# Kernel optimization log

Hardware: AMD Instinct MI355X
Metric: run time of the kernel (lower is better)

Reference implementation:

```python
import jax, jax.numpy as jnp
import numpy as np

T = 2048      # sequence length (block_size)
C = 4096      # n_embd
H = 32        # n_head
KVH = 8       # n_kv_head
D = 128       # head_dim = n_embd // n_head
NEG_INF = -40000.0
ROPE_BASE = 10000.0


def setup_inputs() -> dict:
    key = jax.random.key(0)
    ks = jax.random.split(key, 5)
    x = jax.random.normal(ks[0], (T, C), jnp.float32)
    # nn.Linear weights stored as (in, out); y = x @ W. Small init for numerical sanity.
    Wq = jax.random.normal(ks[1], (C, H * D), jnp.float32) * 0.02
    Wk = jax.random.normal(ks[2], (C, KVH * D), jnp.float32) * 0.02
    Wv = jax.random.normal(ks[3], (C, KVH * D), jnp.float32) * 0.02
    Wo = jax.random.normal(ks[4], (C, C), jnp.float32) * 0.02
    # Standard LLaMA-style RoPE tables: (T, D)
    inv_freq = 1.0 / (ROPE_BASE ** (np.arange(0, D, 2, dtype=np.float32) / D))
    freqs = np.outer(np.arange(T, dtype=np.float32), inv_freq)  # (T, D/2)
    emb = np.concatenate([freqs, freqs], axis=-1)                # (T, D)
    cos = jnp.asarray(np.cos(emb), jnp.float32)
    sin = jnp.asarray(np.sin(emb), jnp.float32)
    # Additive causal mask (T, T): 0 on/below diagonal, neg_inf above.
    causal = np.tril(np.ones((T, T), dtype=bool))
    mask = jnp.where(jnp.asarray(causal), 0.0, NEG_INF).astype(jnp.float32)
    return {"x": x, "Wq": Wq, "Wk": Wk, "Wv": Wv, "Wo": Wo,
            "cos": cos, "sin": sin, "mask": mask}


def _rotate_half(u):
    u1, u2 = jnp.split(u, 2, axis=-1)
    return jnp.concatenate([-u2, u1], axis=-1)


def _apply_rope(u, cos, sin):
    # u: (heads, T, D); cos/sin: (T, D) broadcast over heads
    return u * cos + _rotate_half(u) * sin


def reference(x, Wq, Wk, Wv, Wo, cos, sin, mask):
    Tn = x.shape[0]
    q = (x @ Wq).reshape(Tn, H, D).transpose(1, 0, 2)      # (H, T, D)
    k = (x @ Wk).reshape(Tn, KVH, D).transpose(1, 0, 2)    # (KVH, T, D)
    v = (x @ Wv).reshape(Tn, KVH, D).transpose(1, 0, 2)    # (KVH, T, D)
    q = _apply_rope(q, cos, sin)
    k = _apply_rope(k, cos, sin)
    out_k, out_v = k, v
    # GQA expand: each kv head repeated contiguously H//KVH times
    rep = H // KVH
    ke = jnp.repeat(k, rep, axis=0)                         # (H, T, D)
    ve = jnp.repeat(v, rep, axis=0)                         # (H, T, D)
    # NOTE: no 1/sqrt(D) scaling in the original module
    att = jnp.einsum('htd,hsd->hts', q, ke) + mask          # (H, T, T)
    att = jax.nn.softmax(att, axis=-1)
    y = jnp.einsum('hts,hsd->htd', att, ve)                 # (H, T, D)
    y = y.transpose(1, 0, 2).reshape(Tn, C) @ Wo            # (T, C)
    return (y, out_k, out_v)
```

## Files before the change

### kernel.cpp

```cpp
#include <hip/hip_runtime.h>
#include <hip/hip_bf16.h>

#define T 2048
#define C 4096
#define H 32
#define KVH 8
#define D 128

typedef __bf16 bf16x8 __attribute__((ext_vector_type(8)));
typedef __bf16 bf16x4 __attribute__((ext_vector_type(4)));
typedef float floatx4 __attribute__((ext_vector_type(4)));

#define MFMA16 __builtin_amdgcn_mfma_f32_16x16x32_bf16

__device__ __forceinline__ void gemm_split_body(
    const float* __restrict__ A, const float* __restrict__ B,
    float* __restrict__ Cm, int N, int K, int row0, int col0) {
  __shared__ __bf16 Ah[128][40], Al[128][40], Bh[128][40], Bl[128][40];
  const int tid = threadIdx.x;
  const int lane = tid & 63;
  const int w = tid >> 6;
  const int n16 = lane & 15;
  const int quad = lane >> 4;
  const int wm = w >> 1, wn = w & 1;

  floatx4 acc[4][4];
#pragma unroll
  for (int mi = 0; mi < 4; ++mi)
#pragma unroll
    for (int ni = 0; ni < 4; ++ni) acc[mi][ni] = (floatx4){0.f, 0.f, 0.f, 0.f};

  const int ar = tid >> 3;
  const int ak = (tid & 7) * 4;
  const int bg = tid >> 7;
  const int bn = tid & 127;

  for (int k0 = 0; k0 < K; k0 += 32) {
#pragma unroll
    for (int p = 0; p < 4; ++p) {
      const int r = p * 32 + ar;
      const float4 av = *(const float4*)(A + (size_t)(row0 + r) * K + k0 + ak);
      bf16x4 h, l;
      h[0] = (__bf16)av.x; l[0] = (__bf16)(av.x - (float)h[0]);
      h[1] = (__bf16)av.y; l[1] = (__bf16)(av.y - (float)h[1]);
      h[2] = (__bf16)av.z; l[2] = (__bf16)(av.z - (float)h[2]);
      h[3] = (__bf16)av.w; l[3] = (__bf16)(av.w - (float)h[3]);
      *(bf16x4*)(&Ah[r][ak]) = h;
      *(bf16x4*)(&Al[r][ak]) = l;
    }
#pragma unroll
    for (int p = 0; p < 4; ++p) {
      const int kb = bg * 16 + p * 4;
      const float* bp = B + (size_t)(k0 + kb) * N + col0 + bn;
      const float f0 = bp[0];
      const float f1 = bp[(size_t)N];
      const float f2 = bp[(size_t)2 * N];
      const float f3 = bp[(size_t)3 * N];
      bf16x4 h, l;
      h[0] = (__bf16)f0; l[0] = (__bf16)(f0 - (float)h[0]);
      h[1] = (__bf16)f1; l[1] = (__bf16)(f1 - (float)h[1]);
      h[2] = (__bf16)f2; l[2] = (__bf16)(f2 - (float)h[2]);
      h[3] = (__bf16)f3; l[3] = (__bf16)(f3 - (float)h[3]);
      *(bf16x4*)(&Bh[bn][kb]) = h;
      *(bf16x4*)(&Bl[bn][kb]) = l;
    }
    __syncthreads();
    bf16x8 a_h[4], a_l[4], b_h[4], b_l[4];
#pragma unroll
    for (int mi = 0; mi < 4; ++mi) {
      a_h[mi] = *(const bf16x8*)(&Ah[wm * 64 + mi * 16 + n16][quad * 8]);
      a_l[mi] = *(const bf16x8*)(&Al[wm * 64 + mi * 16 + n16][quad * 8]);
    }
#pragma unroll
    for (int ni = 0; ni < 4; ++ni) {
      b_h[ni] = *(const bf16x8*)(&Bh[wn * 64 + ni * 16 + n16][quad * 8]);
      b_l[ni] = *(const bf16x8*)(&Bl[wn * 64 + ni * 16 + n16][quad * 8]);
    }
#pragma unroll
    for (int mi = 0; mi < 4; ++mi)
#pragma unroll
      for (int ni = 0; ni < 4; ++ni) {
        acc[mi][ni] = MFMA16(a_h[mi], b_h[ni], acc[mi][ni], 0, 0, 0);
        acc[mi][ni] = MFMA16(a_l[mi], b_h[ni], acc[mi][ni], 0, 0, 0);
        acc[mi][ni] = MFMA16(a_h[mi], b_l[ni], acc[mi][ni], 0, 0, 0);
      }
    __syncthreads();
  }
#pragma unroll
  for (int mi = 0; mi < 4; ++mi)
#pragma unroll
    for (int i = 0; i < 4; ++i) {
      const int r = row0 + wm * 64 + mi * 16 + quad * 4 + i;
      float* cp = Cm + (size_t)r * N + col0 + wn * 64 + n16;
#pragma unroll
      for (int ni = 0; ni < 4; ++ni) cp[ni * 16] = acc[mi][ni][i];
    }
}

__global__ __launch_bounds__(256) void gemm_split(
    const float* __restrict__ A, const float* __restrict__ B,
    float* __restrict__ Cm, int N, int K) {
  gemm_split_body(A, B, Cm, N, K, blockIdx.y * 128, blockIdx.x * 128);
}

__global__ __launch_bounds__(256) void gemm_kv(
    const float* __restrict__ A, const float* __restrict__ Bk,
    const float* __restrict__ Bv, float* __restrict__ Ck,
    float* __restrict__ Cv, int K) {
  const int bx = blockIdx.x;
  const float* Bp = (bx < 8) ? Bk : Bv;
  float* Cp = (bx < 8) ? Ck : Cv;
  gemm_split_body(A, Bp, Cp, KVH * D, K, blockIdx.y * 128, (bx & 7) * 128);
}

__global__ __launch_bounds__(256) void rope_kernel(
    float* __restrict__ q, float* __restrict__ k,
    const float* __restrict__ cosb,
    const float* __restrict__ sinb) {
  int idx = blockIdx.x * 256 + threadIdx.x;
  int total = T * (H + KVH) * (D / 2);
  if (idx >= total) return;
  int d = idx % (D / 2);
  int rest = idx / (D / 2);
  int head = rest % (H + KVH);
  int t = rest / (H + KVH);
  float cv = cosb[(size_t)t * D + d];
  float sv = sinb[(size_t)t * D + d];
  float* base;
  if (head < H) base = q + (size_t)t * (H * D) + head * D;
  else          base = k + (size_t)t * (KVH * D) + (head - H) * D;
  float u1 = base[d];
  float u2 = base[d + D / 2];
  base[d]         = u1 * cv - u2 * sv;
  base[d + D / 2] = u2 * cv + u1 * sv;
}

__global__ __launch_bounds__(256) void convert_k(
    const float* __restrict__ k_ws, float* __restrict__ out_k,
    __bf16* __restrict__ khi, __bf16* __restrict__ klo) {
  int idx = blockIdx.x * 256 + threadIdx.x;
  if (idx >= KVH * T * D) return;
  int d = idx & (D - 1);
  int t = (idx >> 7) & (T - 1);
  int kvh = idx >> 18;
  float f = k_ws[(size_t)t * (KVH * D) + kvh * D + d];
  out_k[idx] = f;
  __bf16 hi = (__bf16)f;
  khi[idx] = hi;
  klo[idx] = (__bf16)(f - (float)hi);
}

__global__ __launch_bounds__(256) void convert_v(
    const float* __restrict__ v_ws, float* __restrict__ out_v,
    __bf16* __restrict__ vt) {
  __shared__ __bf16 tile[64][65];
  const int t0 = blockIdx.x * 64;
  const int d0 = blockIdx.y * 64;
  const int kvh = blockIdx.z;
#pragma unroll
  for (int p = 0; p < 16; ++p) {
    int i = p * 256 + threadIdx.x;
    int r = i >> 6;
    int c = i & 63;
    float f = v_ws[(size_t)(t0 + r) * (KVH * D) + kvh * D + d0 + c];
    out_v[((size_t)kvh * T + t0 + r) * D + d0 + c] = f;
    tile[r][c] = (__bf16)f;
  }
  __syncthreads();
#pragma unroll
  for (int p = 0; p < 16; ++p) {
    int i = p * 256 + threadIdx.x;
    int dd = i >> 6;
    int tt = i & 63;
    vt[((size_t)kvh * D + d0 + dd) * T + t0 + tt] = tile[tt][dd];
  }
}

struct StageRegs { bf16x8 k0, k1, l0, l1, v0, v1; };

__device__ __forceinline__ void stage_load(
    StageRegs& s, const __bf16* __restrict__ Kh, const __bf16* __restrict__ Kl,
    const __bf16* __restrict__ Vt, int j0, int tid) {
  const int kr = tid >> 4, kj = (tid & 15) * 8;
  s.k0 = *(const bf16x8*)(Kh + (size_t)(j0 + kr) * D + kj);
  s.k1 = *(const bf16x8*)(Kh + (size_t)(j0 + kr + 16) * D + kj);
  s.l0 = *(const bf16x8*)(Kl + (size_t)(j0 + kr) * D + kj);
  s.l1 = *(const bf16x8*)(Kl + (size_t)(j0 + kr + 16) * D + kj);
  const int vd = tid >> 2, vj = (tid & 3) * 8;
  s.v0 = *(const bf16x8*)(Vt + (size_t)vd * T + j0 + vj);
  s.v1 = *(const bf16x8*)(Vt + (size_t)(vd + 64) * T + j0 + vj);
}

__device__ __forceinline__ void stage_write(
    const StageRegs& s, __bf16* __restrict__ KhL, __bf16* __restrict__ KlL,
    __bf16* __restrict__ VL, int tid) {
  const int kr = tid >> 4, kj = (tid & 15) * 8;
  *(bf16x8*)(KhL + kr * 136 + kj) = s.k0;
  *(bf16x8*)(KhL + (kr + 16) * 136 + kj) = s.k1;
  *(bf16x8*)(KlL + kr * 136 + kj) = s.l0;
  *(bf16x8*)(KlL + (kr + 16) * 136 + kj) = s.l1;
  const int vd = tid >> 2, vj = (tid & 3) * 8;
  *(bf16x8*)(VL + vd * 40 + vj) = s.v0;
  *(bf16x8*)(VL + (vd + 64) * 40 + vj) = s.v1;
}

__device__ __forceinline__ void softmax_pv(
    floatx4 s0, floatx4 s1,
    const __bf16* __restrict__ VT, __bf16* __restrict__ Pw,
    floatx4* __restrict__ O, float* __restrict__ m_i, float* __restrict__ l_i,
    int j0, int r_base, int n16, int quad) {
  if (j0 + 31 > r_base) {
#pragma unroll
    for (int i = 0; i < 4; ++i) {
      int r = r_base + quad * 4 + i;
      if (j0 + n16 > r) s0[i] = -INFINITY;
      if (j0 + 16 + n16 > r) s1[i] = -INFINITY;
    }
  }
  float p0[4], p1[4];
#pragma unroll
  for (int i = 0; i < 4; ++i) {
    float mt = fmaxf(s0[i], s1[i]);
    mt = fmaxf(mt, __shfl_xor(mt, 1));
    mt = fmaxf(mt, __shfl_xor(mt, 2));
    mt = fmaxf(mt, __shfl_xor(mt, 4));
    mt = fmaxf(mt, __shfl_xor(mt, 8));
    float mn = fmaxf(m_i[i], mt);
    float alpha = __expf(m_i[i] - mn);
    m_i[i] = mn;
    p0[i] = __expf(s0[i] - mn);
    p1[i] = __expf(s1[i] - mn);
    float rs = p0[i] + p1[i];
    rs += __shfl_xor(rs, 1);
    rs += __shfl_xor(rs, 2);
    rs += __shfl_xor(rs, 4);
    rs += __shfl_xor(rs, 8);
    l_i[i] = l_i[i] * alpha + rs;
#pragma unroll
    for (int dt = 0; dt < 8; ++dt) O[dt][i] *= alpha;
  }
#pragma unroll
  for (int i = 0; i < 4; ++i) {
    Pw[(quad * 4 + i) * 40 + n16] = (__bf16)p0[i];
    Pw[(quad * 4 + i) * 40 + n16 + 16] = (__bf16)p1[i];
  }
  bf16x8 pA = *(const bf16x8*)(Pw + n16 * 40 + quad * 8);
#pragma unroll
  for (int dt = 0; dt < 8; ++dt) {
    bf16x8 vB = *(const bf16x8*)(VT + (dt * 16 + n16) * 40 + quad * 8);
    O[dt] = MFMA16(pA, vB, O[dt], 0, 0, 0);
  }
}

template <bool BOTH>
__device__ __forceinline__ void attn_tile2(
    const __bf16* __restrict__ KhT, const __bf16* __restrict__ KlT,
    const __bf16* __restrict__ VT, __bf16* __restrict__ Pw,
    const bf16x8* qh_hi, const bf16x8* ql_hi,
    const bf16x8* qh_lo, const bf16x8* ql_lo,
    floatx4* O_hi, float* m_hi, float* l_hi,
    floatx4* O_lo, float* m_lo, float* l_lo,
    int j0, int rb_hi, int rb_lo, int n16, int quad) {
  floatx4 sh0 = {0.f, 0.f, 0.f, 0.f}, sh1 = {0.f, 0.f, 0.f, 0.f};
  floatx4 sl0 = {0.f, 0.f, 0.f, 0.f}, sl1 = {0.f, 0.f, 0.f, 0.f};
#pragma unroll
  for (int c = 0; c < 4; ++c) {
    const int off = c * 32 + quad * 8;
    bf16x8 k0h = *(const bf16x8*)(KhT + n16 * 136 + off);
    bf16x8 k1h = *(const bf16x8*)(KhT + (n16 + 16) * 136 + off);
    bf16x8 k0l = *(const bf16x8*)(KlT + n16 * 136 + off);
    bf16x8 k1l = *(const bf16x8*)(KlT + (n16 + 16) * 136 + off);
    sh0 = MFMA16(qh_hi[c], k0h, sh0, 0, 0, 0);
    sh0 = MFMA16(ql_hi[c], k0h, sh0, 0, 0, 0);
    sh0 = MFMA16(qh_hi[c], k0l, sh0, 0, 0, 0);
    sh1 = MFMA16(qh_hi[c], k1h, sh1, 0, 0, 0);
    sh1 = MFMA16(ql_hi[c], k1h, sh1, 0, 0, 0);
    sh1 = MFMA16(qh_hi[c], k1l, sh1, 0, 0, 0);
    if (BOTH) {
      sl0 = MFMA16(qh_lo[c], k0h, sl0, 0, 0, 0);
      sl0 = MFMA16(ql_lo[c], k0h, sl0, 0, 0, 0);
      sl0 = MFMA16(qh_lo[c], k0l, sl0, 0, 0, 0);
      sl1 = MFMA16(qh_lo[c], k1h, sl1, 0, 0, 0);
      sl1 = MFMA16(ql_lo[c], k1h, sl1, 0, 0, 0);
      sl1 = MFMA16(qh_lo[c], k1l, sl1, 0, 0, 0);
    }
  }
  softmax_pv(sh0, sh1, VT, Pw, O_hi, m_hi, l_hi, j0, rb_hi, n16, quad);
  if (BOTH) softmax_pv(sl0, sl1, VT, Pw, O_lo, m_lo, l_lo, j0, rb_lo, n16, quad);
}

__global__ __launch_bounds__(256, 2) void flash_attn(
    float* __restrict__ q,
    const __bf16* __restrict__ khi,
    const __bf16* __restrict__ klo,
    const __bf16* __restrict__ vt) {
  __shared__ __attribute__((aligned(16))) __bf16 KhL[2][32 * 136];
  __shared__ __attribute__((aligned(16))) __bf16 KlL[2][32 * 136];
  __shared__ __attribute__((aligned(16))) __bf16 VL[2][128 * 40];
  __shared__ __attribute__((aligned(16))) __bf16 Pst[4][16 * 40];

  const int tid = threadIdx.x;
  const int w = tid >> 6;
  const int lane = tid & 63;
  const int n16 = lane & 15;
  const int quad = lane >> 4;
  const int h = blockIdx.y;
  const int kvh = h >> 2;
  const int p_lo = blockIdx.x;
  const int p_hi = 31 - p_lo;
  const int rb_lo = p_lo * 64 + w * 16;
  const int rb_hi = p_hi * 64 + w * 16;
  const int nt = 64 - 2 * p_lo;
  const int nt_lo = (rb_lo + 15) / 32 + 1;
  const int nt_hi = (rb_hi + 15) / 32 + 1;

  const __bf16* Kh = khi + (size_t)kvh * T * D;
  const __bf16* Kl = klo + (size_t)kvh * T * D;
  const __bf16* Vt = vt + (size_t)kvh * D * T;

  bf16x8 qh_lo[4], ql_lo[4], qh_hi[4], ql_hi[4];
  {
    const float* qr_lo = q + (size_t)(rb_lo + n16) * C + h * D;
    const float* qr_hi = q + (size_t)(rb_hi + n16) * C + h * D;
#pragma unroll
    for (int c = 0; c < 4; ++c) {
      const float4 a0 = *(const float4*)(qr_lo + c * 32 + quad * 8);
      const float4 a1 = *(const float4*)(qr_lo + c * 32 + quad * 8 + 4);
      const float4 b0 = *(const float4*)(qr_hi + c * 32 + quad * 8);
      const float4 b1 = *(const float4*)(qr_hi + c * 32 + quad * 8 + 4);
      const float fl[8] = {a0.x, a0.y, a0.z, a0.w, a1.x, a1.y, a1.z, a1.w};
      const float fh[8] = {b0.x, b0.y, b0.z, b0.w, b1.x, b1.y, b1.z, b1.w};
#pragma unroll
      for (int jj = 0; jj < 8; ++jj) {
        __bf16 hl = (__bf16)fl[jj];
        qh_lo[c][jj] = hl;
        ql_lo[c][jj] = (__bf16)(fl[jj] - (float)hl);
        __bf16 hh = (__bf16)fh[jj];
        qh_hi[c][jj] = hh;
        ql_hi[c][jj] = (__bf16)(fh[jj] - (float)hh);
      }
    }
  }

  floatx4 O_lo[8], O_hi[8];
#pragma unroll
  for (int dt = 0; dt < 8; ++dt) {
    O_lo[dt] = (floatx4){0.f, 0.f, 0.f, 0.f};
    O_hi[dt] = (floatx4){0.f, 0.f, 0.f, 0.f};
  }
  float m_lo[4] = {-INFINITY, -INFINITY, -INFINITY, -INFINITY};
  float m_hi[4] = {-INFINITY, -INFINITY, -INFINITY, -INFINITY};
  float l_lo[4] = {0.f, 0.f, 0.f, 0.f};
  float l_hi[4] = {0.f, 0.f, 0.f, 0.f};

  StageRegs sreg;
  stage_load(sreg, Kh, Kl, Vt, 0, tid);
  stage_write(sreg, KhL[0], KlL[0], VL[0], tid);
  __syncthreads();

  __bf16* Pw = Pst[w];
  for (int t = 0; t < nt; ++t) {
    const int cur = t & 1;
    const int j0 = t * 32;
    if (t + 1 < nt) stage_load(sreg, Kh, Kl, Vt, j0 + 32, tid);
    if (t < nt_hi) {
      if (t < nt_lo)
        attn_tile2<true>(KhL[cur], KlL[cur], VL[cur], Pw,
                         qh_hi, ql_hi, qh_lo, ql_lo,
                         O_hi, m_hi, l_hi, O_lo, m_lo, l_lo,
                         j0, rb_hi, rb_lo, n16, quad);
      else
        attn_tile2<false>(KhL[cur], KlL[cur], VL[cur], Pw,
                          qh_hi, ql_hi, qh_lo, ql_lo,
                          O_hi, m_hi, l_hi, O_lo, m_lo, l_lo,
                          j0, rb_hi, rb_lo, n16, quad);
    }
    if (t + 1 < nt) stage_write(sreg, KhL[cur ^ 1], KlL[cur ^ 1], VL[cur ^ 1], tid);
    __syncthreads();
  }

#pragma unroll
  for (int i = 0; i < 4; ++i) {
    float inv_l = 1.0f / l_lo[i];
    float inv_h = 1.0f / l_hi[i];
    int r_l = rb_lo + quad * 4 + i;
    int r_h = rb_hi + quad * 4 + i;
    float* yl = q + (size_t)r_l * C + h * D + n16;
    float* yh = q + (size_t)r_h * C + h * D + n16;
#pragma unroll
    for (int dt = 0; dt < 8; ++dt) {
      yl[dt * 16] = O_lo[dt][i] * inv_l;
      yh[dt * 16] = O_hi[dt][i] * inv_h;
    }
  }
}

extern "C" void kernel_launch(void* const* d_in, const int* in_sizes, int n_in,
                              void* d_out, int out_size, void* d_ws, size_t ws_size,
                              hipStream_t stream) {
  (void)in_sizes; (void)n_in; (void)out_size; (void)ws_size;
  const float* x    = (const float*)d_in[0];
  const float* Wq   = (const float*)d_in[1];
  const float* Wk   = (const float*)d_in[2];
  const float* Wv   = (const float*)d_in[3];
  const float* Wo   = (const float*)d_in[4];
  const float* cosb = (const float*)d_in[5];
  const float* sinb = (const float*)d_in[6];

  float* q_ws = (float*)d_ws;
  float* k_ws = q_ws + (size_t)T * C;
  float* v_ws = k_ws + (size_t)T * KVH * D;
  __bf16* khi = (__bf16*)(v_ws + (size_t)T * KVH * D);
  __bf16* klo = khi + (size_t)KVH * T * D;
  __bf16* vt  = klo + (size_t)KVH * T * D;

  float* out_y = (float*)d_out;
  float* out_k = out_y + (size_t)T * C;
  float* out_v = out_k + (size_t)KVH * T * D;

  dim3 blk(256);
  gemm_split<<<dim3(C / 128, T / 128), blk, 0, stream>>>(x, Wq, q_ws, H * D, C);
  gemm_kv<<<dim3(16, T / 128), blk, 0, stream>>>(x, Wk, Wv, k_ws, v_ws, C);
  int rope_total = T * (H + KVH) * (D / 2);
  rope_kernel<<<(rope_total + 255) / 256, blk, 0, stream>>>(q_ws, k_ws, cosb, sinb);
  convert_k<<<(KVH * T * D) / 256, blk, 0, stream>>>(k_ws, out_k, khi, klo);
  convert_v<<<dim3(T / 64, D / 64, KVH), blk, 0, stream>>>(v_ws, out_v, vt);
  flash_attn<<<dim3(16, H), blk, 0, stream>>>(q_ws, khi, klo, vt);
  gemm_split<<<dim3(C / 128, T / 128), blk, 0, stream>>>(q_ws, Wo, out_y, C, C);
}
```

Before: 957.2 us.

## Fuse QKV GEMMs, drop low-B term in V/O GEMMs, lazy softmax rescale

Merges the Q and KV projection GEMMs into one launch. The V and output projections now use two bf16 split terms instead of three, dropping the low part of B and about a third of their MFMAs. Flash attention skips the running-max rescale unless the new max exceeds the old one by more than 8, and raises wave priority around MFMA sections. Accuracy drops slightly in the V and output GEMMs, and the lazy rescale allows larger intermediate exponents.

```diff
diff --git a/kernel.cpp b/kernel.cpp
--- a/kernel.cpp
+++ b/kernel.cpp
@@ -13,10 +13,12 @@
 
 #define MFMA16 __builtin_amdgcn_mfma_f32_16x16x32_bf16
 
+template <int NTERMS>
 __device__ __forceinline__ void gemm_split_body(
     const float* __restrict__ A, const float* __restrict__ B,
     float* __restrict__ Cm, int N, int K, int row0, int col0) {
-  __shared__ __bf16 Ah[128][40], Al[128][40], Bh[128][40], Bl[128][40];
+  __shared__ __bf16 Ah[128][40], Al[128][40], Bh[128][40];
+  __shared__ __bf16 Bl[NTERMS == 3 ? 128 : 1][NTERMS == 3 ? 40 : 1];
   const int tid = threadIdx.x;
   const int lane = tid & 63;
   const int w = tid >> 6;
@@ -56,13 +58,20 @@
       const float f1 = bp[(size_t)N];
       const float f2 = bp[(size_t)2 * N];
       const float f3 = bp[(size_t)3 * N];
-      bf16x4 h, l;
-      h[0] = (__bf16)f0; l[0] = (__bf16)(f0 - (float)h[0]);
-      h[1] = (__bf16)f1; l[1] = (__bf16)(f1 - (float)h[1]);
-      h[2] = (__bf16)f2; l[2] = (__bf16)(f2 - (float)h[2]);
-      h[3] = (__bf16)f3; l[3] = (__bf16)(f3 - (float)h[3]);
+      bf16x4 h;
+      h[0] = (__bf16)f0;
+      h[1] = (__bf16)f1;
+      h[2] = (__bf16)f2;
+      h[3] = (__bf16)f3;
       *(bf16x4*)(&Bh[bn][kb]) = h;
-      *(bf16x4*)(&Bl[bn][kb]) = l;
+      if constexpr (NTERMS == 3) {
+        bf16x4 l;
+        l[0] = (__bf16)(f0 - (float)h[0]);
+        l[1] = (__bf16)(f1 - (float)h[1]);
+        l[2] = (__bf16)(f2 - (float)h[2]);
+        l[3] = (__bf16)(f3 - (float)h[3]);
+        *(bf16x4*)(&Bl[bn][kb]) = l;
+      }
     }
     __syncthreads();
     bf16x8 a_h[4], a_l[4], b_h[4], b_l[4];
@@ -74,7 +83,8 @@
 #pragma unroll
     for (int ni = 0; ni < 4; ++ni) {
       b_h[ni] = *(const bf16x8*)(&Bh[wn * 64 + ni * 16 + n16][quad * 8]);
-      b_l[ni] = *(const bf16x8*)(&Bl[wn * 64 + ni * 16 + n16][quad * 8]);
+      if constexpr (NTERMS == 3)
+        b_l[ni] = *(const bf16x8*)(&Bl[wn * 64 + ni * 16 + n16][quad * 8]);
     }
 #pragma unroll
     for (int mi = 0; mi < 4; ++mi)
@@ -82,7 +92,8 @@
       for (int ni = 0; ni < 4; ++ni) {
         acc[mi][ni] = MFMA16(a_h[mi], b_h[ni], acc[mi][ni], 0, 0, 0);
         acc[mi][ni] = MFMA16(a_l[mi], b_h[ni], acc[mi][ni], 0, 0, 0);
-        acc[mi][ni] = MFMA16(a_h[mi], b_l[ni], acc[mi][ni], 0, 0, 0);
+        if constexpr (NTERMS == 3)
+          acc[mi][ni] = MFMA16(a_h[mi], b_l[ni], acc[mi][ni], 0, 0, 0);
       }
     __syncthreads();
   }
@@ -97,20 +108,27 @@
     }
 }
 
-__global__ __launch_bounds__(256) void gemm_split(
+template <int NTERMS>
+__global__ __launch_bounds__(256) void gemm_split_t(
     const float* __restrict__ A, const float* __restrict__ B,
     float* __restrict__ Cm, int N, int K) {
-  gemm_split_body(A, B, Cm, N, K, blockIdx.y * 128, blockIdx.x * 128);
-}
-
-__global__ __launch_bounds__(256) void gemm_kv(
-    const float* __restrict__ A, const float* __restrict__ Bk,
-    const float* __restrict__ Bv, float* __restrict__ Ck,
-    float* __restrict__ Cv, int K) {
+  gemm_split_body<NTERMS>(A, B, Cm, N, K, blockIdx.y * 128, blockIdx.x * 128);
+}
+
+__global__ __launch_bounds__(256) void gemm_qkv(
+    const float* __restrict__ x, const float* __restrict__ Wq,
+    const float* __restrict__ Wk, const float* __restrict__ Wv,
+    float* __restrict__ q_ws, float* __restrict__ k_ws,
+    float* __restrict__ v_ws) {
   const int bx = blockIdx.x;
-  const float* Bp = (bx < 8) ? Bk : Bv;
-  float* Cp = (bx < 8) ? Ck : Cv;
-  gemm_split_body(A, Bp, Cp, KVH * D, K, blockIdx.y * 128, (bx & 7) * 128);
+  const int row0 = blockIdx.y * 128;
+  if (bx < 32) {
+    gemm_split_body<3>(x, Wq, q_ws, H * D, C, row0, bx * 128);
+  } else if (bx < 40) {
+    gemm_split_body<3>(x, Wk, k_ws, KVH * D, C, row0, (bx - 32) * 128);
+  } else {
+    gemm_split_body<2>(x, Wv, v_ws, KVH * D, C, row0, (bx - 40) * 128);
+  }
 }
 
 __global__ __launch_bounds__(256) void rope_kernel(
@@ -225,19 +243,21 @@
     mt = fmaxf(mt, __shfl_xor(mt, 2));
     mt = fmaxf(mt, __shfl_xor(mt, 4));
     mt = fmaxf(mt, __shfl_xor(mt, 8));
-    float mn = fmaxf(m_i[i], mt);
-    float alpha = __expf(m_i[i] - mn);
-    m_i[i] = mn;
-    p0[i] = __expf(s0[i] - mn);
-    p1[i] = __expf(s1[i] - mn);
+    if (mt > m_i[i] + 8.0f) {
+      float alpha = __expf(m_i[i] - mt);
+      m_i[i] = mt;
+      l_i[i] *= alpha;
+#pragma unroll
+      for (int dt = 0; dt < 8; ++dt) O[dt][i] *= alpha;
+    }
+    p0[i] = __expf(s0[i] - m_i[i]);
+    p1[i] = __expf(s1[i] - m_i[i]);
     float rs = p0[i] + p1[i];
     rs += __shfl_xor(rs, 1);
     rs += __shfl_xor(rs, 2);
     rs += __shfl_xor(rs, 4);
     rs += __shfl_xor(rs, 8);
-    l_i[i] = l_i[i] * alpha + rs;
-#pragma unroll
-    for (int dt = 0; dt < 8; ++dt) O[dt][i] *= alpha;
+    l_i[i] += rs;
   }
 #pragma unroll
   for (int i = 0; i < 4; ++i) {
@@ -245,11 +265,13 @@
     Pw[(quad * 4 + i) * 40 + n16 + 16] = (__bf16)p1[i];
   }
   bf16x8 pA = *(const bf16x8*)(Pw + n16 * 40 + quad * 8);
+  __builtin_amdgcn_s_setprio(1);
 #pragma unroll
   for (int dt = 0; dt < 8; ++dt) {
     bf16x8 vB = *(const bf16x8*)(VT + (dt * 16 + n16) * 40 + quad * 8);
     O[dt] = MFMA16(pA, vB, O[dt], 0, 0, 0);
   }
+  __builtin_amdgcn_s_setprio(0);
 }
 
 template <bool BOTH>
@@ -263,6 +285,7 @@
     int j0, int rb_hi, int rb_lo, int n16, int quad) {
   floatx4 sh0 = {0.f, 0.f, 0.f, 0.f}, sh1 = {0.f, 0.f, 0.f, 0.f};
   floatx4 sl0 = {0.f, 0.f, 0.f, 0.f}, sl1 = {0.f, 0.f, 0.f, 0.f};
+  __builtin_amdgcn_s_setprio(1);
 #pragma unroll
   for (int c = 0; c < 4; ++c) {
     const int off = c * 32 + quad * 8;
@@ -285,6 +308,7 @@
       sl1 = MFMA16(qh_lo[c], k1l, sl1, 0, 0, 0);
     }
   }
+  __builtin_amdgcn_s_setprio(0);
   softmax_pv(sh0, sh1, VT, Pw, O_hi, m_hi, l_hi, j0, rb_hi, n16, quad);
   if (BOTH) softmax_pv(sl0, sl1, VT, Pw, O_lo, m_lo, l_lo, j0, rb_lo, n16, quad);
 }
@@ -419,12 +443,11 @@
   float* out_v = out_k + (size_t)KVH * T * D;
 
   dim3 blk(256);
-  gemm_split<<<dim3(C / 128, T / 128), blk, 0, stream>>>(x, Wq, q_ws, H * D, C);
-  gemm_kv<<<dim3(16, T / 128), blk, 0, stream>>>(x, Wk, Wv, k_ws, v_ws, C);
+  gemm_qkv<<<dim3(48, T / 128), blk, 0, stream>>>(x, Wq, Wk, Wv, q_ws, k_ws, v_ws);
   int rope_total = T * (H + KVH) * (D / 2);
   rope_kernel<<<(rope_total + 255) / 256, blk, 0, stream>>>(q_ws, k_ws, cosb, sinb);
   convert_k<<<(KVH * T * D) / 256, blk, 0, stream>>>(k_ws, out_k, khi, klo);
   convert_v<<<dim3(T / 64, D / 64, KVH), blk, 0, stream>>>(v_ws, out_v, vt);
   flash_attn<<<dim3(16, H), blk, 0, stream>>>(q_ws, khi, klo, vt);
-  gemm_split<<<dim3(C / 128, T / 128), blk, 0, stream>>>(q_ws, Wo, out_y, C, C);
-}
+  gemm_split_t<2><<<dim3(C / 128, T / 128), blk, 0, stream>>>(q_ws, Wo, out_y, C, C);
+}
```

Result: slower. 1.249 ms (+30.4%).
